# Performance work log

Hardware: AMD Instinct MI355X
Metric: run time of the kernel (lower is better)

## Reference

```python
import jax, jax.numpy as jnp
import numpy as np

NUM_HEADS = 16
WINDOW = 32
HIDDEN = 1024
HEAD_DIM = HIDDEN // NUM_HEADS


def setup_inputs() -> dict:
    key = jax.random.key(0)
    ks = jax.random.split(key, 9)
    B, S, H = 2, 2048, HIDDEN
    s = 0.02
    return {
        "hidden_states": jax.random.normal(ks[0], (B, S, H), jnp.float32),
        "Wq": jax.random.normal(ks[1], (H, H), jnp.float32) * s,
        "bq": jnp.zeros((H,), jnp.float32),
        "Wk": jax.random.normal(ks[2], (H, H), jnp.float32) * s,
        "bk": jnp.zeros((H,), jnp.float32),
        "Wv": jax.random.normal(ks[3], (H, H), jnp.float32) * s,
        "bv": jnp.zeros((H,), jnp.float32),
        "Wo": jax.random.normal(ks[4], (H, H), jnp.float32) * s,
        "bo": jnp.zeros((H,), jnp.float32),
    }


def reference(hidden_states, Wq, bq, Wk, bk, Wv, bv, Wo, bo):
    B, S, H = hidden_states.shape
    scale = jnp.sqrt(jnp.asarray(HEAD_DIM, hidden_states.dtype))
    # torch Linear: x @ W.T + b
    q = (hidden_states @ Wq.T + bq).reshape(B, S, NUM_HEADS, HEAD_DIM)
    k = (hidden_states @ Wk.T + bk).reshape(B, S, NUM_HEADS, HEAD_DIM)
    v = (hidden_states @ Wv.T + bv).reshape(B, S, NUM_HEADS, HEAD_DIM)
    # Full scores; block-causal pattern: query in block bi sees keys in blocks <= bi.
    scores = jnp.einsum("bihd,bjhd->bhij", q, k) / scale  # [B,H,S,S]
    blk = jnp.arange(S) // WINDOW
    allowed = blk[:, None] >= blk[None, :]  # [S,S]
    # Faithful to original: unfilled (future-block) entries are ZERO, not -inf,
    # and still participate in the softmax.
    scores = jnp.where(allowed, scores, jnp.zeros((), scores.dtype))
    probs = jax.nn.softmax(scores, axis=-1)
    ctx = jnp.einsum("bhij,bjhd->bihd", probs, v).reshape(B, S, H)
    return ctx @ Wo.T + bo
```

## Files before the change

### kernel.cpp

```cpp
#include <hip/hip_runtime.h>
#include <cstdint>

namespace {

constexpr int kS   = 2048;
constexpr int kNH  = 16;
constexpr int kHD  = 64;
constexpr int kH   = 1024;
constexpr int kB   = 2;
constexpr int kWin = 32;
constexpr int kNBlk = kS / kWin;
constexpr float kQScale = 0.18033688011112042f;

typedef __attribute__((ext_vector_type(8))) short short8v;
typedef __attribute__((ext_vector_type(4))) float f32x4;
typedef __attribute__((ext_vector_type(4))) unsigned short u16x4;
typedef __attribute__((ext_vector_type(8))) unsigned short u16x8;
typedef __attribute__((ext_vector_type(2))) unsigned int u32x2;

static __device__ __forceinline__ unsigned short f2bf(float f) {
  unsigned int u = __float_as_uint(f);
  return (unsigned short)((u + 0x7fffu + ((u >> 16) & 1u)) >> 16);
}
static __device__ __forceinline__ float bf2f(unsigned short b) {
  return __uint_as_float((unsigned int)b << 16);
}
static __device__ __forceinline__ void async16(const void* g, void* l) {
  __builtin_amdgcn_global_load_lds((__attribute__((address_space(1))) void*)(g),
                                   (__attribute__((address_space(3))) void*)(l),
                                   16, 0, 0);
}

__global__ __launch_bounds__(256) void cvt_bf16(
    const float* __restrict__ hs, const float* __restrict__ Wq,
    const float* __restrict__ Wk, const float* __restrict__ Wv,
    const float* __restrict__ Wo, unsigned short* __restrict__ out)
{
  const size_t idx = ((size_t)blockIdx.x * 256 + threadIdx.x) * 8;
  const int seg = (int)(idx >> 20);
  const size_t off = idx & ((1u << 20) - 1);
  const float* src;
  if (seg < 4)       src = hs + idx;
  else if (seg == 4) src = Wq + off;
  else if (seg == 5) src = Wk + off;
  else if (seg == 6) src = Wv + off;
  else               src = Wo + off;
  const float4 f0 = *(const float4*)(src);
  const float4 f1 = *(const float4*)(src + 4);
  u16x8 pk;
  pk[0] = f2bf(f0.x); pk[1] = f2bf(f0.y); pk[2] = f2bf(f0.z); pk[3] = f2bf(f0.w);
  pk[4] = f2bf(f1.x); pk[5] = f2bf(f1.y); pk[6] = f2bf(f1.z); pk[7] = f2bf(f1.w);
  *(u16x8*)(out + idx) = pk;
}

template <int MT, int EPI>
__global__ __launch_bounds__(256) void gemm_mfma(
    const unsigned short* __restrict__ A, const unsigned short* __restrict__ W,
    const float* __restrict__ b0, const float* __restrict__ b1,
    const float* __restrict__ b2, float* __restrict__ Cf,
    unsigned short* __restrict__ Dq, unsigned short* __restrict__ Dk,
    unsigned short* __restrict__ Dv, int M, int N, int K)
{
  constexpr int BMr = MT * 32;
  __shared__ unsigned short As[BMr * 64];
  __shared__ unsigned short Ws[128 * 64];
  const int tid  = threadIdx.x;
  const int wave = tid >> 6, lane = tid & 63;
  const int q16  = lane & 15, quad = lane >> 4;
  const int wm   = wave & 1,  wn   = wave >> 1;
  const int bm = blockIdx.y * BMr, bn = blockIdx.x * 128;

  const int lrow8 = lane >> 3;
  const int lch   = lane & 7;
  const int gch   = lch ^ lrow8;

  const unsigned short* gA[MT];
  unsigned short* lA[MT];
#pragma unroll
  for (int g = 0; g < MT; ++g) {
    const int row0 = wave * MT * 8 + g * 8;
    gA[g] = A + (size_t)(bm + row0 + lrow8) * K + gch * 8;
    lA[g] = As + row0 * 64;
  }
  const unsigned short* gW[4];
  unsigned short* lW[4];
#pragma unroll
  for (int g = 0; g < 4; ++g) {
    const int row0 = wave * 32 + g * 8;
    gW[g] = W + (size_t)(bn + row0 + lrow8) * K + gch * 8;
    lW[g] = Ws + row0 * 64;
  }

  const unsigned short* fA = As + (wm * (MT * 16) + q16) * 64;
  const unsigned short* fB = Ws + (wn * 64 + q16) * 64;
  const int sl0 = ((quad)     ^ (q16 & 7)) * 8;
  const int sl1 = ((quad + 4) ^ (q16 & 7)) * 8;

  const f32x4 zero = {0.f, 0.f, 0.f, 0.f};
  f32x4 acc[MT][4];
#pragma unroll
  for (int i = 0; i < MT; ++i)
#pragma unroll
    for (int j = 0; j < 4; ++j) acc[i][j] = zero;

  for (int k0 = 0; k0 < K; k0 += 64) {
    __syncthreads();
#pragma unroll
    for (int g = 0; g < MT; ++g) { async16(gA[g], lA[g]); gA[g] += 64; }
#pragma unroll
    for (int g = 0; g < 4; ++g)  { async16(gW[g], lW[g]); gW[g] += 64; }
    __syncthreads();

    short8v a[MT], b[4];
#pragma unroll
    for (int t = 0; t < MT; ++t) a[t] = *(const short8v*)(fA + t * 16 * 64 + sl0);
#pragma unroll
    for (int t = 0; t < 4; ++t)  b[t] = *(const short8v*)(fB + t * 16 * 64 + sl0);
#pragma unroll
    for (int mt = 0; mt < MT; ++mt)
#pragma unroll
      for (int nt = 0; nt < 4; ++nt)
        acc[mt][nt] = __builtin_amdgcn_mfma_f32_16x16x32_bf16(a[mt], b[nt], acc[mt][nt], 0, 0, 0);
#pragma unroll
    for (int t = 0; t < MT; ++t) a[t] = *(const short8v*)(fA + t * 16 * 64 + sl1);
#pragma unroll
    for (int t = 0; t < 4; ++t)  b[t] = *(const short8v*)(fB + t * 16 * 64 + sl1);
#pragma unroll
    for (int mt = 0; mt < MT; ++mt)
#pragma unroll
      for (int nt = 0; nt < 4; ++nt)
        acc[mt][nt] = __builtin_amdgcn_mfma_f32_16x16x32_bf16(a[mt], b[nt], acc[mt][nt], 0, 0, 0);
  }

#pragma unroll
  for (int nt = 0; nt < 4; ++nt) {
    const int col = bn + wn * 64 + nt * 16 + q16;
#pragma unroll
    for (int mt = 0; mt < MT; ++mt) {
      const int row0 = bm + wm * (MT * 16) + mt * 16 + quad * 4;
      const f32x4 av = acc[mt][nt];
      if (EPI == 0) {
        const float bv = b0[col];
#pragma unroll
        for (int r = 0; r < 4; ++r)
          Cf[(size_t)(row0 + r) * N + col] = av[r] + bv;
      } else {
        const int mat = col >> 10, c = col & 1023;
        const int b = row0 >> 11, s0 = row0 & 2047;
        const int h = c >> 6, d = c & 63;
        const size_t bhslot = (size_t)(b * kNH + h);
        if (mat == 0) {
          const float bv = b0[c];
          unsigned short* base = Dq + ((bhslot * kS + s0) * kHD + d);
#pragma unroll
          for (int r = 0; r < 4; ++r) base[(size_t)r * kHD] = f2bf((av[r] + bv) * kQScale);
        } else if (mat == 1) {
          const float bv = b1[c];
          unsigned short* base = Dk + ((bhslot * kS + s0) * kHD + d);
#pragma unroll
          for (int r = 0; r < 4; ++r) base[(size_t)r * kHD] = f2bf(av[r] + bv);
        } else {
          const float bv = b2[c];
          u16x4 pk;
          pk[0] = f2bf(av[0] + bv); pk[1] = f2bf(av[1] + bv);
          pk[2] = f2bf(av[2] + bv); pk[3] = f2bf(av[3] + bv);
          *(u16x4*)(Dv + (bhslot * kHD + d) * kS + s0) = pk;
        }
      }
    }
  }
}

__global__ __launch_bounds__(256) void vprefix_kernel(
    const unsigned short* __restrict__ vt, float* __restrict__ vrest)
{
  __shared__ float bsum[64][64];
  __shared__ float ptot[4][64];
  const int bh = blockIdx.x;
  const int d = threadIdx.x & 63, part = threadIdx.x >> 6;
  const unsigned short* base = vt + ((size_t)bh * kHD + d) * kS;
#pragma unroll 4
  for (int j = 0; j < 16; ++j) {
    const int jb = part * 16 + j;
    const unsigned short* p = base + jb * kWin;
    float s = 0.f;
#pragma unroll
    for (int i = 0; i < 4; ++i) {
      const u16x8 v = *(const u16x8*)(p + i * 8);
#pragma unroll
      for (int e = 0; e < 8; ++e) s += bf2f(v[e]);
    }
    bsum[jb][d] = s;
  }
  __syncthreads();
  float t = 0.f;
#pragma unroll
  for (int j = 0; j < 16; ++j) t += bsum[part * 16 + j][d];
  ptot[part][d] = t;
  __syncthreads();
  float s = 0.f;
  for (int p2 = part + 1; p2 < 4; ++p2) s += ptot[p2][d];
#pragma unroll
  for (int j = 15; j >= 0; --j) {
    const int bi = part * 16 + j;
    vrest[((size_t)bh * kNBlk + bi) * kHD + d] = s;
    s += bsum[bi][d];
  }
}

template <int QT0>
__device__ __forceinline__ void attn_iter(
    const unsigned short* __restrict__ Kb, const unsigned short* __restrict__ Vtb,
    int jb, const short8v qf[4][2], unsigned short* __restrict__ esw,
    int q16, int quad, int swz, f32x4 acc[4][4], float dAcc[4])
{
  short8v vf[4];
#pragma unroll
  for (int nt = 0; nt < 4; ++nt)
    vf[nt] = *(const short8v*)(Vtb + (size_t)(nt * 16 + q16) * kS +
                               jb * kWin + quad * 8);

  const unsigned short* Kj = Kb + (size_t)jb * kWin * kHD;
  short8v kf[2][2];
#pragma unroll
  for (int kt = 0; kt < 2; ++kt)
#pragma unroll
    for (int ks = 0; ks < 2; ++ks)
      kf[kt][ks] = *(const short8v*)(Kj + (kt * 16 + q16) * kHD + ks * 32 + quad * 8);

  const f32x4 zero = {0.f, 0.f, 0.f, 0.f};
#pragma unroll
  for (int kt = 0; kt < 2; ++kt) {
    f32x4 st[4];
#pragma unroll
    for (int qt = QT0; qt < 4; ++qt) {
      f32x4 c = zero;
      c = __builtin_amdgcn_mfma_f32_16x16x32_bf16(kf[kt][0], qf[qt][0], c, 0, 0, 0);
      c = __builtin_amdgcn_mfma_f32_16x16x32_bf16(kf[kt][1], qf[qt][1], c, 0, 0, 0);
      st[qt] = c;
    }
    const int g = kt * 2 + (quad >> 1);
    const int col = ((g ^ swz) * 8) + (quad & 1) * 4;
#pragma unroll
    for (int qt = QT0; qt < 4; ++qt) {
      const float e0 = __builtin_amdgcn_exp2f(st[qt][0]);
      const float e1 = __builtin_amdgcn_exp2f(st[qt][1]);
      const float e2 = __builtin_amdgcn_exp2f(st[qt][2]);
      const float e3 = __builtin_amdgcn_exp2f(st[qt][3]);
      dAcc[qt] += (e0 + e1) + (e2 + e3);
      const unsigned int r0 = __float_as_uint(e0) + 0x8000u;
      const unsigned int r1 = __float_as_uint(e1) + 0x8000u;
      const unsigned int r2 = __float_as_uint(e2) + 0x8000u;
      const unsigned int r3 = __float_as_uint(e3) + 0x8000u;
      u32x2 w;
      w[0] = __builtin_amdgcn_perm(r1, r0, 0x07060302u);
      w[1] = __builtin_amdgcn_perm(r3, r2, 0x07060302u);
      *(u32x2*)(esw + (qt * 16 + q16) * 32 + col) = w;
    }
  }
  short8v af[4];
#pragma unroll
  for (int mt = QT0; mt < 4; ++mt)
    af[mt] = *(const short8v*)(esw + (mt * 16 + q16) * 32 + (quad ^ swz) * 8);
#pragma unroll
  for (int nt = 0; nt < 4; ++nt) {
#pragma unroll
    for (int mt = QT0; mt < 4; ++mt)
      acc[mt][nt] = __builtin_amdgcn_mfma_f32_16x16x32_bf16(af[mt], vf[nt], acc[mt][nt], 0, 0, 0);
  }
}

__global__ __launch_bounds__(256, 3) void attn_mfma(
    const unsigned short* __restrict__ qb, const unsigned short* __restrict__ kb,
    const unsigned short* __restrict__ vtb, const float* __restrict__ vrest,
    unsigned short* __restrict__ ctx)
{
  __shared__ union SM {
    unsigned short es[4][2048];
    struct { float part[2][4096]; float den[4][64]; } m;
  } sm;

  const int tid  = threadIdx.x;
  const int wave = tid >> 6;
  const int lane = tid & 63;
  const int q16  = lane & 15;
  const int quad = lane >> 4;
  const int bh = blockIdx.x & 31;
  const int pr = 31 - (blockIdx.x >> 5);
  const int bilo = pr * 2, bihi = pr * 2 + 1;
  const int b  = bh >> 4, h = bh & 15;

  const unsigned short* Qb  = qb  + ((size_t)bh * kS + (size_t)pr * 64) * kHD;
  const unsigned short* Kb  = kb  + (size_t)bh * kS * kHD;
  const unsigned short* Vtb = vtb + (size_t)bh * kHD * kS;

  short8v qf[4][2];
#pragma unroll
  for (int qt = 0; qt < 4; ++qt)
#pragma unroll
    for (int ks = 0; ks < 2; ++ks)
      qf[qt][ks] = *(const short8v*)(Qb + (qt * 16 + q16) * kHD + ks * 32 + quad * 8);

  const f32x4 zero = {0.f, 0.f, 0.f, 0.f};
  f32x4 acc[4][4];
#pragma unroll
  for (int mt = 0; mt < 4; ++mt)
#pragma unroll
    for (int nt = 0; nt < 4; ++nt) acc[mt][nt] = zero;
  float dAcc[4] = {0.f, 0.f, 0.f, 0.f};

  unsigned short* esw = sm.es[wave];
  const int swz = (q16 >> 2) & 3;

  for (int jb = wave; jb <= bilo; jb += 4)
    attn_iter<0>(Kb, Vtb, jb, qf, esw, q16, quad, swz, acc, dAcc);
  if ((bihi & 3) == wave)
    attn_iter<2>(Kb, Vtb, bihi, qf, esw, q16, quad, swz, acc, dAcc);

#pragma unroll
  for (int qt = 0; qt < 4; ++qt) {
    dAcc[qt] += __shfl_xor(dAcc[qt], 16);
    dAcc[qt] += __shfl_xor(dAcc[qt], 32);
  }

  __syncthreads();
  if (quad == 0) {
#pragma unroll
    for (int qt = 0; qt < 4; ++qt) sm.m.den[wave][qt * 16 + q16] = dAcc[qt];
  }
  if (wave < 2) {
    float* p = sm.m.part[wave];
#pragma unroll
    for (int mt = 0; mt < 4; ++mt)
#pragma unroll
      for (int nt = 0; nt < 4; ++nt)
#pragma unroll
        for (int r = 0; r < 4; ++r)
          p[((mt * 4 + nt) * 4 + r) * 64 + lane] = acc[mt][nt][r];
  }
  __syncthreads();
  if (wave >= 2) {
    float* p = sm.m.part[wave - 2];
#pragma unroll
    for (int mt = 0; mt < 4; ++mt)
#pragma unroll
      for (int nt = 0; nt < 4; ++nt)
#pragma unroll
        for (int r = 0; r < 4; ++r)
          p[((mt * 4 + nt) * 4 + r) * 64 + lane] += acc[mt][nt][r];
  }
  __syncthreads();

  {
    const int nt = wave;
    const int dim = nt * 16 + q16;
    const float vrlo = vrest[((size_t)bh * kNBlk + bilo) * kHD + dim];
    const float vrhi = vrest[((size_t)bh * kNBlk + bihi) * kHD + dim];
    const float nrlo = 32.0f * (float)((kNBlk - 1) - bilo);
    const float nrhi = 32.0f * (float)((kNBlk - 1) - bihi);
    unsigned short* outb = ctx + ((size_t)b * kS + (size_t)pr * 64) * kH + h * kHD;
#pragma unroll
    for (int mt = 0; mt < 4; ++mt) {
      const float vr = (mt < 2) ? vrlo : vrhi;
      const float nr = (mt < 2) ? nrlo : nrhi;
#pragma unroll
      for (int r = 0; r < 4; ++r) {
        const int idx = ((mt * 4 + nt) * 4 + r) * 64 + lane;
        const int qrow = mt * 16 + quad * 4 + r;
        const float den = sm.m.den[0][qrow] + sm.m.den[1][qrow] +
                          sm.m.den[2][qrow] + sm.m.den[3][qrow] + nr;
        outb[(size_t)qrow * kH + dim] =
            f2bf((sm.m.part[0][idx] + sm.m.part[1][idx] + vr) / den);
      }
    }
  }
}

}

extern "C" void kernel_launch(void* const* d_in, const int* in_sizes, int n_in,
                              void* d_out, int out_size, void* d_ws, size_t ws_size,
                              hipStream_t stream) {
  const float* hs = (const float*)d_in[0];
  const float* Wq = (const float*)d_in[1];
  const float* bq = (const float*)d_in[2];
  const float* Wk = (const float*)d_in[3];
  const float* bk = (const float*)d_in[4];
  const float* Wv = (const float*)d_in[5];
  const float* bv = (const float*)d_in[6];
  const float* Wo = (const float*)d_in[7];
  const float* bo = (const float*)d_in[8];

  char* wsb = (char*)d_ws;
  unsigned short* hsb   = (unsigned short*)(wsb);
  unsigned short* wqkv  = hsb + (4u << 20);
  unsigned short* wob   = hsb + (7u << 20);
  unsigned short* qbuf  = (unsigned short*)(wsb + (16u << 20));
  unsigned short* kbuf  = (unsigned short*)(wsb + (24u << 20));
  unsigned short* vtbuf = (unsigned short*)(wsb + (32u << 20));
  unsigned short* ctxb  = (unsigned short*)(wsb + (40u << 20));
  float*          vrest = (float*)         (wsb + (48u << 20));

  const int M = kB * kS;

  cvt_bf16<<<4096, 256, 0, stream>>>(hs, Wq, Wk, Wv, Wo, hsb);
  gemm_mfma<4, 1><<<dim3(3072 / 128, M / 128), 256, 0, stream>>>(
      hsb, wqkv, bq, bk, bv, nullptr, qbuf, kbuf, vtbuf, M, 3072, kH);
  vprefix_kernel<<<kB * kNH, 256, 0, stream>>>(vtbuf, vrest);
  attn_mfma<<<(kNBlk / 2) * kB * kNH, 256, 0, stream>>>(qbuf, kbuf, vtbuf, vrest, ctxb);
  gemm_mfma<2, 0><<<dim3(kH / 128, M / 64), 256, 0, stream>>>(
      ctxb, wob, bo, nullptr, nullptr, (float*)d_out, nullptr, nullptr, nullptr,
      M, kH, kH);
}
```

Before: 202.9 us.

## Double-buffer V tiles via async LDS loads and prefetch next K fragments

Measured after the change: 252.5 us. 1.24x slower.

```diff
diff --git a/kernel.cpp b/kernel.cpp
--- a/kernel.cpp
+++ b/kernel.cpp
@@ -208,41 +208,54 @@
   }
 }
 
-template <int QT0>
-__device__ __forceinline__ void attn_iter(
-    const unsigned short* __restrict__ Kb, const unsigned short* __restrict__ Vtb,
-    int jb, const short8v qf[4][2], unsigned short* __restrict__ esw,
-    int q16, int quad, int swz, f32x4 acc[4][4], float dAcc[4])
-{
-  short8v vf[4];
-#pragma unroll
-  for (int nt = 0; nt < 4; ++nt)
-    vf[nt] = *(const short8v*)(Vtb + (size_t)(nt * 16 + q16) * kS +
-                               jb * kWin + quad * 8);
-
+__device__ __forceinline__ void load_kf(short8v kf[2][2],
+    const unsigned short* __restrict__ Kb, int jb, int q16, int quad) {
   const unsigned short* Kj = Kb + (size_t)jb * kWin * kHD;
-  short8v kf[2][2];
 #pragma unroll
   for (int kt = 0; kt < 2; ++kt)
 #pragma unroll
     for (int ks = 0; ks < 2; ++ks)
       kf[kt][ks] = *(const short8v*)(Kj + (kt * 16 + q16) * kHD + ks * 32 + quad * 8);
-
+}
+
+__device__ __forceinline__ void dma_vtile(const unsigned short* __restrict__ Vtb,
+    int jb, unsigned short* __restrict__ lbuf, int lane) {
+  const int rl = lane >> 2;
+  const int g  = (lane & 3) ^ ((rl >> 1) & 3);
+#pragma unroll
+  for (int c = 0; c < 4; ++c) {
+    const int row = c * 16 + rl;
+    async16(Vtb + (size_t)row * kS + jb * kWin + g * 8, lbuf + c * 512);
+  }
+}
+
+__device__ __forceinline__ void attn_step(
+    const unsigned short* __restrict__ Kb, const unsigned short* __restrict__ Vtb,
+    int jb, bool hn, const short8v qf[4][2],
+    const short8v kfc[2][2], short8v kfn[2][2],
+    const unsigned short* __restrict__ vcur, unsigned short* __restrict__ vnxt,
+    unsigned short* __restrict__ esw,
+    int q16, int quad, int lane, int swz, f32x4 acc[4][4], float dAcc[4])
+{
+  if (hn) {
+    dma_vtile(Vtb, jb + 4, vnxt, lane);
+    load_kf(kfn, Kb, jb + 4, q16, quad);
+  }
   const f32x4 zero = {0.f, 0.f, 0.f, 0.f};
 #pragma unroll
   for (int kt = 0; kt < 2; ++kt) {
     f32x4 st[4];
 #pragma unroll
-    for (int qt = QT0; qt < 4; ++qt) {
+    for (int qt = 0; qt < 4; ++qt) {
       f32x4 c = zero;
-      c = __builtin_amdgcn_mfma_f32_16x16x32_bf16(kf[kt][0], qf[qt][0], c, 0, 0, 0);
-      c = __builtin_amdgcn_mfma_f32_16x16x32_bf16(kf[kt][1], qf[qt][1], c, 0, 0, 0);
+      c = __builtin_amdgcn_mfma_f32_16x16x32_bf16(kfc[kt][0], qf[qt][0], c, 0, 0, 0);
+      c = __builtin_amdgcn_mfma_f32_16x16x32_bf16(kfc[kt][1], qf[qt][1], c, 0, 0, 0);
       st[qt] = c;
     }
     const int g = kt * 2 + (quad >> 1);
     const int col = ((g ^ swz) * 8) + (quad & 1) * 4;
 #pragma unroll
-    for (int qt = QT0; qt < 4; ++qt) {
+    for (int qt = 0; qt < 4; ++qt) {
       const float e0 = __builtin_amdgcn_exp2f(st[qt][0]);
       const float e1 = __builtin_amdgcn_exp2f(st[qt][1]);
       const float e2 = __builtin_amdgcn_exp2f(st[qt][2]);
@@ -260,13 +273,67 @@
   }
   short8v af[4];
 #pragma unroll
-  for (int mt = QT0; mt < 4; ++mt)
+  for (int mt = 0; mt < 4; ++mt)
     af[mt] = *(const short8v*)(esw + (mt * 16 + q16) * 32 + (quad ^ swz) * 8);
+  if (hn) __builtin_amdgcn_s_waitcnt(0x0F78);
+  else    __builtin_amdgcn_s_waitcnt(0x0F70);
+  const int vslot = (quad ^ ((q16 >> 1) & 3)) * 8;
 #pragma unroll
   for (int nt = 0; nt < 4; ++nt) {
-#pragma unroll
-    for (int mt = QT0; mt < 4; ++mt)
-      acc[mt][nt] = __builtin_amdgcn_mfma_f32_16x16x32_bf16(af[mt], vf[nt], acc[mt][nt], 0, 0, 0);
+    const short8v vfv = *(const short8v*)(vcur + (nt * 16 + q16) * 32 + vslot);
+#pragma unroll
+    for (int mt = 0; mt < 4; ++mt)
+      acc[mt][nt] = __builtin_amdgcn_mfma_f32_16x16x32_bf16(af[mt], vfv, acc[mt][nt], 0, 0, 0);
+  }
+}
+
+__device__ __forceinline__ void attn_half(
+    const unsigned short* __restrict__ Kb, const unsigned short* __restrict__ Vtb,
+    int jb, const short8v qf[4][2], unsigned short* __restrict__ esw,
+    int q16, int quad, int swz, f32x4 acc[4][4], float dAcc[4])
+{
+  short8v vf[4];
+#pragma unroll
+  for (int nt = 0; nt < 4; ++nt)
+    vf[nt] = *(const short8v*)(Vtb + (size_t)(nt * 16 + q16) * kS + jb * kWin + quad * 8);
+  short8v kf[2][2];
+  load_kf(kf, Kb, jb, q16, quad);
+  const f32x4 zero = {0.f, 0.f, 0.f, 0.f};
+#pragma unroll
+  for (int kt = 0; kt < 2; ++kt) {
+    f32x4 st[4];
+#pragma unroll
+    for (int qt = 2; qt < 4; ++qt) {
+      f32x4 c = zero;
+      c = __builtin_amdgcn_mfma_f32_16x16x32_bf16(kf[kt][0], qf[qt][0], c, 0, 0, 0);
+      c = __builtin_amdgcn_mfma_f32_16x16x32_bf16(kf[kt][1], qf[qt][1], c, 0, 0, 0);
+      st[qt] = c;
+    }
+    const int g = kt * 2 + (quad >> 1);
+    const int col = ((g ^ swz) * 8) + (quad & 1) * 4;
+#pragma unroll
+    for (int qt = 2; qt < 4; ++qt) {
+      const float e0 = __builtin_amdgcn_exp2f(st[qt][0]);
+      const float e1 = __builtin_amdgcn_exp2f(st[qt][1]);
+      const float e2 = __builtin_amdgcn_exp2f(st[qt][2]);
+      const float e3 = __builtin_amdgcn_exp2f(st[qt][3]);
+      dAcc[qt] += (e0 + e1) + (e2 + e3);
+      const unsigned int r0 = __float_as_uint(e0) + 0x8000u;
+      const unsigned int r1 = __float_as_uint(e1) + 0x8000u;
+      const unsigned int r2 = __float_as_uint(e2) + 0x8000u;
+      const unsigned int r3 = __float_as_uint(e3) + 0x8000u;
+      u32x2 w;
+      w[0] = __builtin_amdgcn_perm(r1, r0, 0x07060302u);
+      w[1] = __builtin_amdgcn_perm(r3, r2, 0x07060302u);
+      *(u32x2*)(esw + (qt * 16 + q16) * 32 + col) = w;
+    }
+  }
+#pragma unroll
+  for (int mt = 2; mt < 4; ++mt) {
+    const short8v af = *(const short8v*)(esw + (mt * 16 + q16) * 32 + (quad ^ swz) * 8);
+#pragma unroll
+    for (int nt = 0; nt < 4; ++nt)
+      acc[mt][nt] = __builtin_amdgcn_mfma_f32_16x16x32_bf16(af, vf[nt], acc[mt][nt], 0, 0, 0);
   }
 }
 
@@ -276,7 +343,10 @@
     unsigned short* __restrict__ ctx)
 {
   __shared__ union SM {
-    unsigned short es[4][2048];
+    struct {
+      unsigned short es[4][2048];
+      unsigned short vt[4][2][2048];
+    } a;
     struct { float part[2][4096]; float den[4][64]; } m;
   } sm;
 
@@ -309,13 +379,28 @@
     for (int nt = 0; nt < 4; ++nt) acc[mt][nt] = zero;
   float dAcc[4] = {0.f, 0.f, 0.f, 0.f};
 
-  unsigned short* esw = sm.es[wave];
+  unsigned short* esw = sm.a.es[wave];
+  unsigned short* v0  = sm.a.vt[wave][0];
+  unsigned short* v1  = sm.a.vt[wave][1];
   const int swz = (q16 >> 2) & 3;
 
-  for (int jb = wave; jb <= bilo; jb += 4)
-    attn_iter<0>(Kb, Vtb, jb, qf, esw, q16, quad, swz, acc, dAcc);
+  int jb = wave;
+  short8v kf0[2][2], kf1[2][2];
+  if (jb <= bilo) {
+    dma_vtile(Vtb, jb, v0, lane);
+    load_kf(kf0, Kb, jb, q16, quad);
+  }
+  while (jb <= bilo) {
+    const bool hnA = (jb + 4) <= bilo;
+    attn_step(Kb, Vtb, jb, hnA, qf, kf0, kf1, v0, v1, esw, q16, quad, lane, swz, acc, dAcc);
+    jb += 4;
+    if (jb > bilo) break;
+    const bool hnB = (jb + 4) <= bilo;
+    attn_step(Kb, Vtb, jb, hnB, qf, kf1, kf0, v1, v0, esw, q16, quad, lane, swz, acc, dAcc);
+    jb += 4;
+  }
   if ((bihi & 3) == wave)
-    attn_iter<2>(Kb, Vtb, bihi, qf, esw, q16, quad, swz, acc, dAcc);
+    attn_half(Kb, Vtb, bihi, qf, esw, q16, quad, swz, acc, dAcc);
 
 #pragma unroll
   for (int qt = 0; qt < 4; ++qt) {
```
